# Performance work log

Hardware: AMD Instinct MI355X
Metric: run time of the kernel (lower is better)

The kernel has to match this reference:

```python
import jax, jax.numpy as jnp
import numpy as np
from jax import lax

DN = ('NCHW', 'OIHW', 'NCHW')


def conv3x3(x, w, b):
    return lax.conv_general_dilated(x, w, (1, 1), 'SAME', dimension_numbers=DN) + b[None, :, None, None]


def conv1x1(x, w, b):
    # w: [O, I] -> pointwise conv
    return jnp.einsum('oi,bihw->bohw', w, x) + b[None, :, None, None]


def sft(x0, x1, sc0w, sc0b, sc1w, sc1b, sh0w, sh0b, sh1w, sh1b):
    scale = conv1x1(jax.nn.leaky_relu(conv1x1(x1, sc0w, sc0b), 0.1), sc1w, sc1b)
    shift = conv1x1(jax.nn.leaky_relu(conv1x1(x1, sh0w, sh0b), 0.1), sh1w, sh1b)
    return x0 * (scale + 1.0) + shift


def deform_conv(x, offset, w, b):
    # torchvision DeformConv2d, 3x3, stride 1, pad 1, dilation 1, no mask.
    B, C, H, W = x.shape
    O = w.shape[0]
    K = 9
    off = offset.reshape(B, K, 2, H, W)  # (dy, dx) per kernel tap
    ki = jnp.arange(3, dtype=x.dtype) - 1.0
    ky = jnp.repeat(ki, 3)  # [9]
    kx = jnp.tile(ki, 3)
    hh = jnp.arange(H, dtype=x.dtype)
    ww = jnp.arange(W, dtype=x.dtype)
    py = off[:, :, 0] + hh[None, None, :, None] + ky[None, :, None, None]  # [B,K,H,W]
    px = off[:, :, 1] + ww[None, None, None, :] + kx[None, :, None, None]
    y0f = jnp.floor(py)
    x0f = jnp.floor(px)
    wy = (py - y0f)[:, None]  # [B,1,K,H,W]
    wx = (px - x0f)[:, None]
    y0 = y0f.astype(jnp.int32)
    x0i = x0f.astype(jnp.int32)
    x_flat = x.reshape(B, C, H * W)

    def gather(iy, ix):
        valid = (iy >= 0) & (iy < H) & (ix >= 0) & (ix < W)
        idx = (jnp.clip(iy, 0, H - 1) * W + jnp.clip(ix, 0, W - 1)).reshape(B, K * H * W)
        vals = jax.vmap(lambda xf, ii: xf[:, ii])(x_flat, idx)  # [B,C,K*H*W]
        return vals.reshape(B, C, K, H, W) * valid[:, None].astype(x.dtype)

    v00 = gather(y0, x0i)
    v01 = gather(y0, x0i + 1)
    v10 = gather(y0 + 1, x0i)
    v11 = gather(y0 + 1, x0i + 1)
    samp = (v00 * (1 - wy) * (1 - wx) + v01 * (1 - wy) * wx
            + v10 * wy * (1 - wx) + v11 * wy * wx)  # [B,C,K,H,W]
    return jnp.einsum('bckhw,ock->bohw', samp, w.reshape(O, C, K)) + b[None, :, None, None]


def setup_inputs() -> dict:
    key = jax.random.key(0)
    ks = jax.random.split(key, 32)
    B, C0, C1, H, W = 4, 128, 32, 96, 96
    f32 = jnp.float32
    d = {
        'x0': jax.random.normal(ks[0], (B, C0, H, W), f32),
        'x1': jax.random.normal(ks[1], (B, C1, H, W), f32),
        'w_off': jax.random.normal(ks[2], (18, C0, 3, 3), f32) * 0.02,
        'b_off': jnp.zeros((18,), f32),
        's1_sc0_w': jax.random.normal(ks[3], (C0, C1), f32) * 0.05,
        's1_sc0_b': jnp.zeros((C0,), f32),
        's1_sc1_w': jax.random.normal(ks[4], (C0, C0), f32) * 0.05,
        's1_sc1_b': jnp.zeros((C0,), f32),
        's1_sh0_w': jax.random.normal(ks[5], (C0, C1), f32) * 0.05,
        's1_sh0_b': jnp.zeros((C0,), f32),
        's1_sh1_w': jax.random.normal(ks[6], (C0, C0), f32) * 0.05,
        's1_sh1_b': jnp.zeros((C0,), f32),
        'w_d1': jax.random.normal(ks[7], (C0, C0, 3, 3), f32) * 0.03,
        'b_d1': jnp.zeros((C0,), f32),
        's2_sc0_w': jax.random.normal(ks[8], (C0, C1), f32) * 0.05,
        's2_sc0_b': jnp.zeros((C0,), f32),
        's2_sc1_w': jax.random.normal(ks[9], (C0, C0), f32) * 0.05,
        's2_sc1_b': jnp.zeros((C0,), f32),
        's2_sh0_w': jax.random.normal(ks[10], (C0, C1), f32) * 0.05,
        's2_sh0_b': jnp.zeros((C0,), f32),
        's2_sh1_w': jax.random.normal(ks[11], (C0, C0), f32) * 0.05,
        's2_sh1_b': jnp.zeros((C0,), f32),
        'w_d2': jax.random.normal(ks[12], (C0, C0, 3, 3), f32) * 0.03,
        'b_d2': jnp.zeros((C0,), f32),
    }
    return d


def reference(x0, x1, w_off, b_off,
              s1_sc0_w, s1_sc0_b, s1_sc1_w, s1_sc1_b,
              s1_sh0_w, s1_sh0_b, s1_sh1_w, s1_sh1_b,
              w_d1, b_d1,
              s2_sc0_w, s2_sc0_b, s2_sc1_w, s2_sc1_b,
              s2_sh0_w, s2_sh0_b, s2_sh1_w, s2_sh1_b,
              w_d2, b_d2):
    off = conv3x3(x0, w_off, b_off)
    fea = sft(x0, x1, s1_sc0_w, s1_sc0_b, s1_sc1_w, s1_sc1_b,
              s1_sh0_w, s1_sh0_b, s1_sh1_w, s1_sh1_b)
    fea = jax.nn.relu(deform_conv(fea, off, w_d1, b_d1))
    fea = sft(fea, x1, s2_sc0_w, s2_sc0_b, s2_sc1_w, s2_sc1_b,
              s2_sh0_w, s2_sh0_b, s2_sh1_w, s2_sh1_b)
    fea = deform_conv(fea, off, w_d2, b_d2)
    return x0 + fea
```

## Files before the change

### kernel.cpp

```cpp
#include <hip/hip_runtime.h>

typedef unsigned short u16;
typedef unsigned int   u32;
typedef __attribute__((ext_vector_type(8))) _Float16 f16x8;
typedef __attribute__((ext_vector_type(2))) float f32x2;
typedef __attribute__((ext_vector_type(4))) float f32x4;
typedef __attribute__((ext_vector_type(4))) unsigned int u32x4;

constexpr int B_  = 4;
constexpr int C0  = 128;
constexpr int C1  = 32;
constexpr int H_  = 96;
constexpr int W_  = 96;
constexpr int HW  = H_ * W_;
constexpr int PT  = 64;
constexpr int TPB = HW / PT;
constexpr int NTILE = B_ * TPB;

__device__ inline u16 f2h(float f) {
    _Float16 h = (_Float16)f;
    return __builtin_bit_cast(u16, h);
}

__global__ __launch_bounds__(256) void k_prep(
    const float* __restrict__ w_off,
    const float* __restrict__ wd1,  const float* __restrict__ wd2,
    const float* __restrict__ s1c0, const float* __restrict__ s1h0,
    const float* __restrict__ s2c0, const float* __restrict__ s2h0,
    const float* __restrict__ s1c1, const float* __restrict__ s1h1,
    const float* __restrict__ s2c1, const float* __restrict__ s2h1,
    float* __restrict__ wofft, u16* __restrict__ wdhi, u16* __restrict__ wdlo,
    u16* __restrict__ w0h,     u16* __restrict__ w1h)
{
    int t = blockIdx.x * 256 + threadIdx.x;
    if (t < C0 * 18 * 9) {
        int c = t / 162, r = t % 162, o = r / 9, tap = r % 9;
        wofft[t] = w_off[(o * C0 + c) * 9 + tap];
    }
    if (t < 2 * 9 * C0 * C0) {
        int d = t / (9 * C0 * C0), r = t % (9 * C0 * C0);
        int k = r / (C0 * C0), r2 = r % (C0 * C0), o = r2 / C0, c = r2 % C0;
        const float* wsrc = d ? wd2 : wd1;
        float wv = wsrc[(o * C0 + c) * 9 + k];
        _Float16 hi = (_Float16)wv;
        float rr = wv - (float)hi;
        wdhi[t] = __builtin_bit_cast(u16, hi);
        wdlo[t] = f2h(rr);
    }
    if (t < 4 * C0 * C1) {
        int m = t / (C0 * C1), i = t % (C0 * C1);
        const float* s = (m == 0) ? s1c0 : (m == 1) ? s1h0 : (m == 2) ? s2c0 : s2h0;
        w0h[t] = f2h(s[i]);
    }
    if (t < 4 * C0 * C0) {
        int m = t / (C0 * C0), i = t % (C0 * C0);
        const float* s = (m == 0) ? s1c1 : (m == 1) ? s1h1 : (m == 2) ? s2c1 : s2h1;
        w1h[t] = f2h(s[i]);
    }
}

__global__ __launch_bounds__(256) void k_conv_off(
    const float* __restrict__ x0, const float* __restrict__ wofft,
    const float* __restrict__ boff, float* __restrict__ off)
{
    int bx = blockIdx.x;
    int b  = bx / TPB;
    int p0 = (bx % TPB) * PT;
    int tid = threadIdx.x;
    int p   = tid & 63;
    int cq  = __builtin_amdgcn_readfirstlane(tid >> 6);
    int pos = p0 + p;
    int h = pos / W_, w = pos % W_;

    float acc[18];
#pragma unroll
    for (int o = 0; o < 18; ++o) acc[o] = 0.f;

    for (int cc = 0; cc < 32; ++cc) {
        int c = cq * 32 + cc;
        const float* xb = x0 + ((size_t)(b * C0 + c)) * HW;
        float v[9];
#pragma unroll
        for (int t = 0; t < 9; ++t) {
            int dy = t / 3 - 1, dx = t % 3 - 1;
            int hy = h + dy, wx = w + dx;
            bool ok = (hy >= 0) & (hy < H_) & (wx >= 0) & (wx < W_);
            v[t] = ok ? xb[hy * W_ + wx] : 0.f;
        }
        const float* wr = wofft + c * 162;
#pragma unroll
        for (int o = 0; o < 18; ++o)
#pragma unroll
            for (int t = 0; t < 9; ++t)
                acc[o] = fmaf(wr[o * 9 + t], v[t], acc[o]);
    }

    __shared__ float red[4][18][PT];
#pragma unroll
    for (int o = 0; o < 18; ++o) red[cq][o][p] = acc[o];
    __syncthreads();
    for (int idx = tid; idx < 18 * PT; idx += 256) {
        int o = idx / PT, pp = idx % PT;
        float s = red[0][o][pp] + red[1][o][pp] + red[2][o][pp] + red[3][o][pp]
                + boff[o];
        off[((size_t)(b * 18 + o)) * HW + p0 + pp] = s;
    }
}

template <int XSRC>
__global__ __launch_bounds__(512) void k_sft_mma(
    const float* __restrict__ xf,
    const float* __restrict__ xT,
    const float* __restrict__ x1,
    const u16* __restrict__ w0s, const u16* __restrict__ w0h,
    const u16* __restrict__ w1s, const u16* __restrict__ w1h,
    const float* __restrict__ b0s, const float* __restrict__ b0h,
    const float* __restrict__ b1s, const float* __restrict__ b1h,
    float* __restrict__ outT)
{
    __shared__ __align__(16) u16   x1t[64 * 32];
    __shared__ __align__(16) u16   hidt[2][64 * 128];
    __shared__ __align__(16) float outt[64 * 128];

    int bx = blockIdx.x, b = bx / TPB, p0 = (bx % TPB) * PT;
    int tid = threadIdx.x, l = tid & 63;
    int w = __builtin_amdgcn_readfirstlane(tid >> 6);
    f32x4 zz = {0.f, 0.f, 0.f, 0.f};

    for (int i = tid; i < C1 * PT; i += 512) {
        int ch = i >> 6, pos = i & 63;
        float v = x1[((size_t)(b * C1 + ch)) * HW + p0 + pos];
        x1t[pos * 32 + (ch ^ ((pos & 3) << 3))] = f2h(v);
    }
    __syncthreads();

    {
        int mt = w & 3, br = w >> 2;
        int pos = mt * 16 + (l & 15);
        int koff = (l >> 4) * 8;
        f16x8 a = *(const f16x8*)&x1t[pos * 32 + (koff ^ ((pos & 3) << 3))];
        const u16* w0 = br ? w0h : w0s;
        const float* bb = br ? b0h : b0s;
        u16* hrow = hidt[br];
#pragma unroll
        for (int nt = 0; nt < 8; ++nt) {
            int n = nt * 16 + (l & 15);
            f16x8 bfr = *(const f16x8*)&w0[n * 32 + koff];
            f32x4 h = __builtin_amdgcn_mfma_f32_16x16x32_f16(a, bfr, zz, 0, 0, 0);
            float bv = bb[n];
#pragma unroll
            for (int r = 0; r < 4; ++r) {
                float hv = h[r] + bv;
                hv = hv > 0.f ? hv : 0.1f * hv;
                int prow = mt * 16 + (l >> 4) * 4 + r;
                hrow[prow * 128 + (n ^ ((prow & 7) << 3))] = f2h(hv);
            }
        }
    }
    __syncthreads();

    f32x4 accS[4], accH[4];
#pragma unroll
    for (int nt = 0; nt < 4; ++nt) { accS[nt] = zz; accH[nt] = zz; }
    int mt = w & 3, nh = w >> 2;
    int pos = mt * 16 + (l & 15);
#pragma unroll
    for (int ks = 0; ks < 4; ++ks) {
        int kb = ks * 32 + (l >> 4) * 8;
        f16x8 aS = *(const f16x8*)&hidt[0][pos * 128 + (kb ^ ((pos & 7) << 3))];
        f16x8 aH = *(const f16x8*)&hidt[1][pos * 128 + (kb ^ ((pos & 7) << 3))];
#pragma unroll
        for (int nt = 0; nt < 4; ++nt) {
            int n = nh * 64 + nt * 16 + (l & 15);
            f16x8 bS = *(const f16x8*)&w1s[n * 128 + kb];
            f16x8 bH = *(const f16x8*)&w1h[n * 128 + kb];
            accS[nt] = __builtin_amdgcn_mfma_f32_16x16x32_f16(aS, bS, accS[nt], 0, 0, 0);
            accH[nt] = __builtin_amdgcn_mfma_f32_16x16x32_f16(aH, bH, accH[nt], 0, 0, 0);
        }
    }

#pragma unroll
    for (int nt = 0; nt < 4; ++nt) {
        int n = nh * 64 + nt * 16 + (l & 15);
        float scb = b1s[n], shb = b1h[n];
        float xv[4];
        if (XSRC == 0) {
            const float* xp = xf + ((size_t)(b * C0 + n)) * HW + p0 + mt * 16 + (l >> 4) * 4;
            f32x4 x4 = *(const f32x4*)xp;
#pragma unroll
            for (int r = 0; r < 4; ++r) xv[r] = x4[r];
        } else {
#pragma unroll
            for (int r = 0; r < 4; ++r)
                xv[r] = xT[((size_t)(b * HW + p0 + mt * 16 + (l >> 4) * 4 + r)) * C0 + n];
        }
#pragma unroll
        for (int r = 0; r < 4; ++r) {
            float scale = accS[nt][r] + scb + 1.f;
            float shift = accH[nt][r] + shb;
            outt[(mt * 16 + (l >> 4) * 4 + r) * 128 + n] = xv[r] * scale + shift;
        }
    }
    __syncthreads();

    float* dst = outT + ((size_t)(b * HW + p0)) * C0;
    for (int i = tid; i < 2048; i += 512)
        *(f32x4*)&dst[i * 4] = *(const f32x4*)&outt[i * 4];
}

template <int MODE>
__global__ __launch_bounds__(512) void k_deform3(
    const float* __restrict__ srcT,
    const float* __restrict__ off,
    const u16* __restrict__ whi,
    const u16* __restrict__ wlo,
    const float* __restrict__ bias,
    const float* __restrict__ x0,
    float* __restrict__ outF,
    float* __restrict__ outT)
{
    __shared__ __align__(16) u16 sm[4][64 * 128];
    u16* a_hi = sm[0];  u16* a_lo = sm[1];
    u16* b_hi = sm[2];  u16* b_lo = sm[3];

    int bx = blockIdx.x;
    bx = (bx & 7) * (NTILE / 8) + (bx >> 3);
    int b = bx / TPB, p0 = (bx % TPB) * PT;
    int tid = threadIdx.x, l = tid & 63;
    int w = __builtin_amdgcn_readfirstlane(tid >> 6);
    f32x4 zz = {0.f, 0.f, 0.f, 0.f};

    f32x4 acc[2][2];
#pragma unroll
    for (int hf = 0; hf < 2; ++hf)
#pragma unroll
        for (int nt = 0; nt < 2; ++nt) acc[hf][nt] = zz;

    int mt = w & 3, ng = w >> 2;
    int pos_r = mt * 16 + (l & 15);
    const float* base = srcT + (size_t)b * HW * C0;
    int so = tid >> 3, sp = tid & 7;

    for (int k = 0; k < 9; ++k) {
        for (int i = 0; i < 8; ++i) {
            int pp = w * 8 + i;
            int pos = p0 + pp;
            int h = pos / W_, wc = pos % W_;
            float dy = off[((size_t)(b * 18 + 2 * k)) * HW + pos];
            float dx = off[((size_t)(b * 18 + 2 * k + 1)) * HW + pos];
            float py = dy + (float)(h + k / 3 - 1);
            float px = dx + (float)(wc + k % 3 - 1);
            float yf = floorf(py), xf = floorf(px);
            int y0 = (int)yf, x0i = (int)xf;
            float wy = py - yf, wx = px - xf;
            bool vy0 = (y0 >= 0) & (y0 < H_), vy1 = (y0 + 1 >= 0) & (y0 + 1 < H_);
            bool vx0 = (x0i >= 0) & (x0i < W_), vx1 = (x0i + 1 >= 0) & (x0i + 1 < W_);
            float w00 = (vy0 & vx0) ? (1.f - wy) * (1.f - wx) : 0.f;
            float w01 = (vy0 & vx1) ? (1.f - wy) * wx         : 0.f;
            float w10 = (vy1 & vx0) ? wy * (1.f - wx)         : 0.f;
            float w11 = (vy1 & vx1) ? wy * wx                 : 0.f;
            int iy0 = min(max(y0, 0), H_ - 1), iy1 = min(max(y0 + 1, 0), H_ - 1);
            int ix0 = min(max(x0i, 0), W_ - 1), ix1 = min(max(x0i + 1, 0), W_ - 1);
            const float* q00 = base + (size_t)(iy0 * W_ + ix0) * C0 + 2 * l;
            const float* q01 = base + (size_t)(iy0 * W_ + ix1) * C0 + 2 * l;
            const float* q10 = base + (size_t)(iy1 * W_ + ix0) * C0 + 2 * l;
            const float* q11 = base + (size_t)(iy1 * W_ + ix1) * C0 + 2 * l;
            f32x2 v00 = *(const f32x2*)q00;
            f32x2 v01 = *(const f32x2*)q01;
            f32x2 v10 = *(const f32x2*)q10;
            f32x2 v11 = *(const f32x2*)q11;
            float s0 = v00[0] * w00 + v01[0] * w01 + v10[0] * w10 + v11[0] * w11;
            float s1 = v00[1] * w00 + v01[1] * w01 + v10[1] * w10 + v11[1] * w11;
            _Float16 h0 = (_Float16)s0, h1 = (_Float16)s1;
            float r0 = s0 - (float)h0, r1 = s1 - (float)h1;
            u32 hv = (u32)__builtin_bit_cast(u16, h0) | ((u32)__builtin_bit_cast(u16, h1) << 16);
            u32 lv = (u32)f2h(r0) | ((u32)f2h(r1) << 16);
            int ci = (2 * l) ^ ((pp & 7) << 3);
            *(u32*)&a_hi[pp * 128 + ci] = hv;
            *(u32*)&a_lo[pp * 128 + ci] = lv;
        }

#pragma unroll
        for (int hf = 0; hf < 2; ++hf) {
            {
                int orow = hf * 64 + so;
                const u16* sh = whi + ((size_t)k * C0 + orow) * C0 + sp * 16;
                const u16* sl = wlo + ((size_t)k * C0 + orow) * C0 + sp * 16;
                int sw = (so & 7) << 3;
#pragma unroll
                for (int j = 0; j < 2; ++j) {
                    int cj = (sp * 16 + j * 8) ^ sw;
                    *(u32x4*)&b_hi[so * 128 + cj] = *(const u32x4*)&sh[j * 8];
                    *(u32x4*)&b_lo[so * 128 + cj] = *(const u32x4*)&sl[j * 8];
                }
            }
            __syncthreads();
#pragma unroll
            for (int ks = 0; ks < 4; ++ks) {
                int kb = ks * 32 + (l >> 4) * 8;
                int ai = pos_r * 128 + (kb ^ ((pos_r & 7) << 3));
                f16x8 ah = *(const f16x8*)&a_hi[ai];
                f16x8 al = *(const f16x8*)&a_lo[ai];
#pragma unroll
                for (int nt = 0; nt < 2; ++nt) {
                    int orow = ng * 32 + nt * 16 + (l & 15);
                    int bi = orow * 128 + (kb ^ ((orow & 7) << 3));
                    f16x8 bh = *(const f16x8*)&b_hi[bi];
                    f16x8 bl = *(const f16x8*)&b_lo[bi];
                    acc[hf][nt] = __builtin_amdgcn_mfma_f32_16x16x32_f16(ah, bh, acc[hf][nt], 0, 0, 0);
                    acc[hf][nt] = __builtin_amdgcn_mfma_f32_16x16x32_f16(al, bh, acc[hf][nt], 0, 0, 0);
                    acc[hf][nt] = __builtin_amdgcn_mfma_f32_16x16x32_f16(ah, bl, acc[hf][nt], 0, 0, 0);
                }
            }
            __syncthreads();
        }
    }

    if (MODE == 0) {
        float* otile = (float*)sm;
#pragma unroll
        for (int hf = 0; hf < 2; ++hf)
#pragma unroll
            for (int nt = 0; nt < 2; ++nt) {
                int o = hf * 64 + ng * 32 + nt * 16 + (l & 15);
                float bv = bias[o];
#pragma unroll
                for (int r = 0; r < 4; ++r) {
                    float v = acc[hf][nt][r] + bv;
                    v = v > 0.f ? v : 0.f;
                    otile[(mt * 16 + (l >> 4) * 4 + r) * 128 + o] = v;
                }
            }
        __syncthreads();
        float* dst = outT + ((size_t)(b * HW + p0)) * C0;
        for (int i = tid; i < 2048; i += 512)
            *(f32x4*)&dst[i * 4] = *(const f32x4*)&otile[i * 4];
    } else {
#pragma unroll
        for (int hf = 0; hf < 2; ++hf)
#pragma unroll
            for (int nt = 0; nt < 2; ++nt) {
                int o = hf * 64 + ng * 32 + nt * 16 + (l & 15);
                float bv = bias[o];
                size_t base_o = ((size_t)(b * C0 + o)) * HW + p0 + mt * 16 + (l >> 4) * 4;
                f32x4 x4 = *(const f32x4*)(x0 + base_o);
                f32x4 ov;
#pragma unroll
                for (int r = 0; r < 4; ++r) ov[r] = acc[hf][nt][r] + bv + x4[r];
                *(f32x4*)(outF + base_o) = ov;
            }
    }
}

constexpr size_t WB_OFF   = 0;
constexpr size_t WB_WOFFT = 2654208;
constexpr size_t WB_W0H   = 2737152;
constexpr size_t WB_W1H   = 2769920;
constexpr size_t WB_WDHI  = 2900992;
constexpr size_t WB_WDLO  = 4080640;
constexpr size_t WB_TA    = 5260288;
constexpr size_t WB_TB    = 24134656;

extern "C" void kernel_launch(void* const* d_in, const int* in_sizes, int n_in,
                              void* d_out, int out_size, void* d_ws, size_t ws_size,
                              hipStream_t stream)
{
    const float* x0      = (const float*)d_in[0];
    const float* x1      = (const float*)d_in[1];
    const float* w_off   = (const float*)d_in[2];
    const float* b_off   = (const float*)d_in[3];
    const float* s1_sc0w = (const float*)d_in[4];
    const float* s1_sc0b = (const float*)d_in[5];
    const float* s1_sc1w = (const float*)d_in[6];
    const float* s1_sc1b = (const float*)d_in[7];
    const float* s1_sh0w = (const float*)d_in[8];
    const float* s1_sh0b = (const float*)d_in[9];
    const float* s1_sh1w = (const float*)d_in[10];
    const float* s1_sh1b = (const float*)d_in[11];
    const float* w_d1    = (const float*)d_in[12];
    const float* b_d1    = (const float*)d_in[13];
    const float* s2_sc0w = (const float*)d_in[14];
    const float* s2_sc0b = (const float*)d_in[15];
    const float* s2_sc1w = (const float*)d_in[16];
    const float* s2_sc1b = (const float*)d_in[17];
    const float* s2_sh0w = (const float*)d_in[18];
    const float* s2_sh0b = (const float*)d_in[19];
    const float* s2_sh1w = (const float*)d_in[20];
    const float* s2_sh1b = (const float*)d_in[21];
    const float* w_d2    = (const float*)d_in[22];
    const float* b_d2    = (const float*)d_in[23];

    char* wsb = (char*)d_ws;
    float* off   = (float*)(wsb + WB_OFF);
    float* wofft = (float*)(wsb + WB_WOFFT);
    u16*   w0h   = (u16*)(wsb + WB_W0H);
    u16*   w1h   = (u16*)(wsb + WB_W1H);
    u16*   wdhi  = (u16*)(wsb + WB_WDHI);
    u16*   wdlo  = (u16*)(wsb + WB_WDLO);
    float* TA    = (float*)(wsb + WB_TA);
    float* TB    = (float*)(wsb + WB_TB);

    k_prep<<<1152, 256, 0, stream>>>(w_off, w_d1, w_d2,
                                     s1_sc0w, s1_sh0w, s2_sc0w, s2_sh0w,
                                     s1_sc1w, s1_sh1w, s2_sc1w, s2_sh1w,
                                     wofft, wdhi, wdlo, w0h, w1h);
    k_conv_off<<<NTILE, 256, 0, stream>>>(x0, wofft, b_off, off);
    k_sft_mma<0><<<NTILE, 512, 0, stream>>>(x0, nullptr, x1,
                                            w0h, w0h + 4096,
                                            w1h, w1h + 16384,
                                            s1_sc0b, s1_sh0b, s1_sc1b, s1_sh1b, TA);
    k_deform3<0><<<NTILE, 512, 0, stream>>>(TA, off, wdhi, wdlo, b_d1,
                                            nullptr, nullptr, TB);
    k_sft_mma<1><<<NTILE, 512, 0, stream>>>(nullptr, TB, x1,
                                            w0h + 8192, w0h + 12288,
                                            w1h + 32768, w1h + 49152,
                                            s2_sc0b, s2_sh0b, s2_sc1b, s2_sh1b, TA);
    k_deform3<1><<<NTILE, 512, 0, stream>>>(TA, off, wdhi + 9 * 16384, wdlo + 9 * 16384,
                                            b_d2, x0, (float*)d_out, nullptr);
}
```

Before: 402.3 us.

## Precompute deform sampling indices and prefetch next tap's gathers during MFMA

The deformable conv kernel now precomputes bilinear corner indices, validity flags and fractional weights for all 9 taps into shared memory once per tile. The gathers for the next tap are issued into registers before the current tap's MFMA work, so global gather latency overlaps with matrix math. The XOR swizzle is replaced by padded row strides (136 halves, 132 floats) to avoid LDS bank conflicts, and launch bounds request 4 waves per SIMD. The cost is heavier register use (64 float2 prefetch values per thread) and more LDS per block, which can reduce occupancy or cause spills.

Result: faster. 373.3 us (-7.2%).

```diff
diff --git a/kernel.cpp b/kernel.cpp
--- a/kernel.cpp
+++ b/kernel.cpp
@@ -209,7 +209,7 @@
 }
 
 template <int MODE>
-__global__ __launch_bounds__(512) void k_deform3(
+__global__ __launch_bounds__(512, 4) void k_deform4(
     const float* __restrict__ srcT,
     const float* __restrict__ off,
     const u16* __restrict__ whi,
@@ -219,9 +219,14 @@
     float* __restrict__ outF,
     float* __restrict__ outT)
 {
-    __shared__ __align__(16) u16 sm[4][64 * 128];
-    u16* a_hi = sm[0];  u16* a_lo = sm[1];
-    u16* b_hi = sm[2];  u16* b_lo = sm[3];
+    constexpr int S = 136;
+    __shared__ __align__(16) u16   smem[4 * 64 * S];
+    __shared__ __align__(16) u16   cidx[9 * 64 * 4];
+    __shared__ __align__(16) float cwt[9 * 64 * 2];
+    u16* a_hi = smem;
+    u16* a_lo = smem + 64 * S;
+    u16* b_hi = smem + 2 * 64 * S;
+    u16* b_lo = smem + 3 * 64 * S;
 
     int bx = blockIdx.x;
     bx = (bx & 7) * (NTILE / 8) + (bx >> 3);
@@ -230,6 +235,28 @@
     int w = __builtin_amdgcn_readfirstlane(tid >> 6);
     f32x4 zz = {0.f, 0.f, 0.f, 0.f};
 
+    for (int e = tid; e < 9 * 64; e += 512) {
+        int k = e >> 6, pp = e & 63;
+        int pos = p0 + pp, h = pos / W_, wc = pos % W_;
+        float dy = off[((size_t)(b * 18 + 2 * k)) * HW + pos];
+        float dx = off[((size_t)(b * 18 + 2 * k + 1)) * HW + pos];
+        float py = dy + (float)(h + k / 3 - 1);
+        float px = dx + (float)(wc + k % 3 - 1);
+        float yf = floorf(py), xf = floorf(px);
+        int y0 = (int)yf, x0i = (int)xf;
+        cwt[e * 2]     = py - yf;
+        cwt[e * 2 + 1] = px - xf;
+        int iy0 = min(max(y0, 0), H_ - 1),     iy1 = min(max(y0 + 1, 0), H_ - 1);
+        int ix0 = min(max(x0i, 0), W_ - 1),    ix1 = min(max(x0i + 1, 0), W_ - 1);
+        bool vy0 = (y0 >= 0) & (y0 < H_),      vy1 = (y0 + 1 >= 0) & (y0 + 1 < H_);
+        bool vx0 = (x0i >= 0) & (x0i < W_),    vx1 = (x0i + 1 >= 0) & (x0i + 1 < W_);
+        cidx[e * 4 + 0] = (u16)(iy0 * W_ + ix0) | ((vy0 & vx0) ? 0x8000 : 0);
+        cidx[e * 4 + 1] = (u16)(iy0 * W_ + ix1) | ((vy0 & vx1) ? 0x8000 : 0);
+        cidx[e * 4 + 2] = (u16)(iy1 * W_ + ix0) | ((vy1 & vx0) ? 0x8000 : 0);
+        cidx[e * 4 + 3] = (u16)(iy1 * W_ + ix1) | ((vy1 & vx1) ? 0x8000 : 0);
+    }
+    __syncthreads();
+
     f32x4 acc[2][2];
 #pragma unroll
     for (int hf = 0; hf < 2; ++hf)
@@ -238,86 +265,108 @@
 
     int mt = w & 3, ng = w >> 2;
     int pos_r = mt * 16 + (l & 15);
-    const float* base = srcT + (size_t)b * HW * C0;
     int so = tid >> 3, sp = tid & 7;
-
+    const float* base  = srcT + (size_t)b * HW * C0;
+    const float* lbase = base + 2 * l;
+
+    f32x2 gv[8][4];
+
+#define ISSUE(KK)                                                             \
+    {                                                                         \
+        int ek = (KK) * 64 + w * 8;                                           \
+        _Pragma("unroll")                                                     \
+        for (int i = 0; i < 8; ++i) {                                         \
+            int e = ek + i;                                                   \
+            u32 c01 = *(const u32*)&cidx[e * 4];                              \
+            u32 c23 = *(const u32*)&cidx[e * 4 + 2];                          \
+            gv[i][0] = *(const f32x2*)(lbase + (size_t)(c01 & 0x3fffu) * C0); \
+            gv[i][1] = *(const f32x2*)(lbase + (size_t)((c01 >> 16) & 0x3fffu) * C0); \
+            gv[i][2] = *(const f32x2*)(lbase + (size_t)(c23 & 0x3fffu) * C0); \
+            gv[i][3] = *(const f32x2*)(lbase + (size_t)((c23 >> 16) & 0x3fffu) * C0); \
+        }                                                                     \
+    }
+
+#define COMMIT(KK)                                                            \
+    {                                                                         \
+        int ek = (KK) * 64 + w * 8;                                           \
+        _Pragma("unroll")                                                     \
+        for (int i = 0; i < 8; ++i) {                                         \
+            int e = ek + i, pp = w * 8 + i;                                   \
+            u32 c01 = *(const u32*)&cidx[e * 4];                              \
+            u32 c23 = *(const u32*)&cidx[e * 4 + 2];                          \
+            float wy = cwt[e * 2], wx = cwt[e * 2 + 1];                       \
+            float aa  = wy * wx;                                              \
+            float w11 = (c23 & 0x80000000u) ? aa : 0.f;                       \
+            float w10 = (c23 & 0x8000u) ? (wy - aa) : 0.f;                    \
+            float w01 = (c01 & 0x80000000u) ? (wx - aa) : 0.f;                \
+            float w00 = (c01 & 0x8000u) ? (1.f - wy - wx + aa) : 0.f;         \
+            float s0 = gv[i][0][0] * w00 + gv[i][1][0] * w01                  \
+                     + gv[i][2][0] * w10 + gv[i][3][0] * w11;                 \
+            float s1 = gv[i][0][1] * w00 + gv[i][1][1] * w01                  \
+                     + gv[i][2][1] * w10 + gv[i][3][1] * w11;                 \
+            _Float16 h0 = (_Float16)s0, h1 = (_Float16)s1;                    \
+            float r0 = s0 - (float)h0, r1 = s1 - (float)h1;                   \
+            u32 hv = (u32)__builtin_bit_cast(u16, h0)                         \
+                   | ((u32)__builtin_bit_cast(u16, h1) << 16);                \
+            u32 lv = (u32)f2h(r0) | ((u32)f2h(r1) << 16);                     \
+            *(u32*)&a_hi[pp * S + 2 * l] = hv;                                \
+            *(u32*)&a_lo[pp * S + 2 * l] = lv;                                \
+        }                                                                     \
+    }
+
+#define STAGEB(KK, HF)                                                        \
+    {                                                                         \
+        int orow = (HF) * 64 + so;                                            \
+        const u16* sh = whi + ((size_t)(KK) * C0 + orow) * C0 + sp * 16;      \
+        const u16* sl = wlo + ((size_t)(KK) * C0 + orow) * C0 + sp * 16;      \
+        _Pragma("unroll")                                                     \
+        for (int j = 0; j < 2; ++j) {                                         \
+            *(u32x4*)&b_hi[so * S + sp * 16 + j * 8] = *(const u32x4*)&sh[j * 8]; \
+            *(u32x4*)&b_lo[so * S + sp * 16 + j * 8] = *(const u32x4*)&sl[j * 8]; \
+        }                                                                     \
+    }
+
+#define MFMA_HALF(HF)                                                         \
+    {                                                                         \
+        _Pragma("unroll")                                                     \
+        for (int ks = 0; ks < 4; ++ks) {                                      \
+            int kb = ks * 32 + (l >> 4) * 8;                                  \
+            int ai = pos_r * S + kb;                                          \
+            f16x8 ah = *(const f16x8*)&a_hi[ai];                              \
+            f16x8 al = *(const f16x8*)&a_lo[ai];                              \
+            _Pragma("unroll")                                                 \
+            for (int nt = 0; nt < 2; ++nt) {                                  \
+                int orow = ng * 32 + nt * 16 + (l & 15);                      \
+                int bi = orow * S + kb;                                       \
+                f16x8 bh = *(const f16x8*)&b_hi[bi];                          \
+                f16x8 bl = *(const f16x8*)&b_lo[bi];                          \
+                acc[HF][nt] = __builtin_amdgcn_mfma_f32_16x16x32_f16(ah, bh, acc[HF][nt], 0, 0, 0); \
+                acc[HF][nt] = __builtin_amdgcn_mfma_f32_16x16x32_f16(al, bh, acc[HF][nt], 0, 0, 0); \
+                acc[HF][nt] = __builtin_amdgcn_mfma_f32_16x16x32_f16(ah, bl, acc[HF][nt], 0, 0, 0); \
+            }                                                                 \
+        }                                                                     \
+    }
+
+    ISSUE(0)
     for (int k = 0; k < 9; ++k) {
-        for (int i = 0; i < 8; ++i) {
-            int pp = w * 8 + i;
-            int pos = p0 + pp;
-            int h = pos / W_, wc = pos % W_;
-            float dy = off[((size_t)(b * 18 + 2 * k)) * HW + pos];
-            float dx = off[((size_t)(b * 18 + 2 * k + 1)) * HW + pos];
-            float py = dy + (float)(h + k / 3 - 1);
-            float px = dx + (float)(wc + k % 3 - 1);
-            float yf = floorf(py), xf = floorf(px);
-            int y0 = (int)yf, x0i = (int)xf;
-            float wy = py - yf, wx = px - xf;
-            bool vy0 = (y0 >= 0) & (y0 < H_), vy1 = (y0 + 1 >= 0) & (y0 + 1 < H_);
-            bool vx0 = (x0i >= 0) & (x0i < W_), vx1 = (x0i + 1 >= 0) & (x0i + 1 < W_);
-            float w00 = (vy0 & vx0) ? (1.f - wy) * (1.f - wx) : 0.f;
-            float w01 = (vy0 & vx1) ? (1.f - wy) * wx         : 0.f;
-            float w10 = (vy1 & vx0) ? wy * (1.f - wx)         : 0.f;
-            float w11 = (vy1 & vx1) ? wy * wx                 : 0.f;
-            int iy0 = min(max(y0, 0), H_ - 1), iy1 = min(max(y0 + 1, 0), H_ - 1);
-            int ix0 = min(max(x0i, 0), W_ - 1), ix1 = min(max(x0i + 1, 0), W_ - 1);
-            const float* q00 = base + (size_t)(iy0 * W_ + ix0) * C0 + 2 * l;
-            const float* q01 = base + (size_t)(iy0 * W_ + ix1) * C0 + 2 * l;
-            const float* q10 = base + (size_t)(iy1 * W_ + ix0) * C0 + 2 * l;
-            const float* q11 = base + (size_t)(iy1 * W_ + ix1) * C0 + 2 * l;
-            f32x2 v00 = *(const f32x2*)q00;
-            f32x2 v01 = *(const f32x2*)q01;
-            f32x2 v10 = *(const f32x2*)q10;
-            f32x2 v11 = *(const f32x2*)q11;
-            float s0 = v00[0] * w00 + v01[0] * w01 + v10[0] * w10 + v11[0] * w11;
-            float s1 = v00[1] * w00 + v01[1] * w01 + v10[1] * w10 + v11[1] * w11;
-            _Float16 h0 = (_Float16)s0, h1 = (_Float16)s1;
-            float r0 = s0 - (float)h0, r1 = s1 - (float)h1;
-            u32 hv = (u32)__builtin_bit_cast(u16, h0) | ((u32)__builtin_bit_cast(u16, h1) << 16);
-            u32 lv = (u32)f2h(r0) | ((u32)f2h(r1) << 16);
-            int ci = (2 * l) ^ ((pp & 7) << 3);
-            *(u32*)&a_hi[pp * 128 + ci] = hv;
-            *(u32*)&a_lo[pp * 128 + ci] = lv;
-        }
-
-#pragma unroll
-        for (int hf = 0; hf < 2; ++hf) {
-            {
-                int orow = hf * 64 + so;
-                const u16* sh = whi + ((size_t)k * C0 + orow) * C0 + sp * 16;
-                const u16* sl = wlo + ((size_t)k * C0 + orow) * C0 + sp * 16;
-                int sw = (so & 7) << 3;
-#pragma unroll
-                for (int j = 0; j < 2; ++j) {
-                    int cj = (sp * 16 + j * 8) ^ sw;
-                    *(u32x4*)&b_hi[so * 128 + cj] = *(const u32x4*)&sh[j * 8];
-                    *(u32x4*)&b_lo[so * 128 + cj] = *(const u32x4*)&sl[j * 8];
-                }
-            }
-            __syncthreads();
-#pragma unroll
-            for (int ks = 0; ks < 4; ++ks) {
-                int kb = ks * 32 + (l >> 4) * 8;
-                int ai = pos_r * 128 + (kb ^ ((pos_r & 7) << 3));
-                f16x8 ah = *(const f16x8*)&a_hi[ai];
-                f16x8 al = *(const f16x8*)&a_lo[ai];
-#pragma unroll
-                for (int nt = 0; nt < 2; ++nt) {
-                    int orow = ng * 32 + nt * 16 + (l & 15);
-                    int bi = orow * 128 + (kb ^ ((orow & 7) << 3));
-                    f16x8 bh = *(const f16x8*)&b_hi[bi];
-                    f16x8 bl = *(const f16x8*)&b_lo[bi];
-                    acc[hf][nt] = __builtin_amdgcn_mfma_f32_16x16x32_f16(ah, bh, acc[hf][nt], 0, 0, 0);
-                    acc[hf][nt] = __builtin_amdgcn_mfma_f32_16x16x32_f16(al, bh, acc[hf][nt], 0, 0, 0);
-                    acc[hf][nt] = __builtin_amdgcn_mfma_f32_16x16x32_f16(ah, bl, acc[hf][nt], 0, 0, 0);
-                }
-            }
-            __syncthreads();
-        }
-    }
+        COMMIT(k)
+        STAGEB(k, 0)
+        __syncthreads();
+        if (k < 8) ISSUE(k + 1)
+        MFMA_HALF(0)
+        __syncthreads();
+        STAGEB(k, 1)
+        __syncthreads();
+        MFMA_HALF(1)
+        __syncthreads();
+    }
+#undef ISSUE
+#undef COMMIT
+#undef STAGEB
+#undef MFMA_HALF
 
     if (MODE == 0) {
-        float* otile = (float*)sm;
+        float* otile = (float*)smem;
 #pragma unroll
         for (int hf = 0; hf < 2; ++hf)
 #pragma unroll
@@ -328,13 +377,15 @@
                 for (int r = 0; r < 4; ++r) {
                     float v = acc[hf][nt][r] + bv;
                     v = v > 0.f ? v : 0.f;
-                    otile[(mt * 16 + (l >> 4) * 4 + r) * 128 + o] = v;
+                    otile[(mt * 16 + (l >> 4) * 4 + r) * 132 + o] = v;
                 }
             }
         __syncthreads();
         float* dst = outT + ((size_t)(b * HW + p0)) * C0;
-        for (int i = tid; i < 2048; i += 512)
-            *(f32x4*)&dst[i * 4] = *(const f32x4*)&otile[i * 4];
+        for (int i = tid; i < 2048; i += 512) {
+            int row = i >> 5, c = i & 31;
+            *(f32x4*)&dst[row * 128 + c * 4] = *(const f32x4*)&otile[row * 132 + c * 4];
+        }
     } else {
 #pragma unroll
         for (int hf = 0; hf < 2; ++hf)
@@ -409,12 +460,12 @@
                                             w0h, w0h + 4096,
                                             w1h, w1h + 16384,
                                             s1_sc0b, s1_sh0b, s1_sc1b, s1_sh1b, TA);
-    k_deform3<0><<<NTILE, 512, 0, stream>>>(TA, off, wdhi, wdlo, b_d1,
+    k_deform4<0><<<NTILE, 512, 0, stream>>>(TA, off, wdhi, wdlo, b_d1,
                                             nullptr, nullptr, TB);
     k_sft_mma<1><<<NTILE, 512, 0, stream>>>(nullptr, TB, x1,
                                             w0h + 8192, w0h + 12288,
                                             w1h + 32768, w1h + 49152,
                                             s2_sc0b, s2_sh0b, s2_sc1b, s2_sh1b, TA);
-    k_deform3<1><<<NTILE, 512, 0, stream>>>(TA, off, wdhi + 9 * 16384, wdlo + 9 * 16384,
+    k_deform4<1><<<NTILE, 512, 0, stream>>>(TA, off, wdhi + 9 * 16384, wdlo + 9 * 16384,
                                             b_d2, x0, (float*)d_out, nullptr);
 }
```

## Cut LDS use in deform and SFT kernels to raise occupancy

Applied to the files above, without the earlier changes.

The deform kernel no longer stages weights in LDS; MFMA B operands are read straight from global (L2-cached) memory. Sampling indices, validity bits and fractional weights are precomputed once per tile into LDS. Each wave now covers 64 output channels, and padded strides replace XOR swizzles. The SFT kernel drops its output staging tile and writes directly to global memory. Both kernels get launch bounds of 6 waves per SIMD. The aim is lower LDS and register pressure so more blocks fit per CU. The risk is heavier global traffic for weights and uncoalesced SFT stores.

Measured after the change: 636.7 us. 58.3% more time.

```diff
diff --git a/kernel.cpp b/kernel.cpp
--- a/kernel.cpp
+++ b/kernel.cpp
@@ -108,7 +108,7 @@
 }
 
 template <int XSRC>
-__global__ __launch_bounds__(512) void k_sft_mma(
+__global__ __launch_bounds__(512, 6) void k_sft_mma(
     const float* __restrict__ xf,
     const float* __restrict__ xT,
     const float* __restrict__ x1,
@@ -118,9 +118,8 @@
     const float* __restrict__ b1s, const float* __restrict__ b1h,
     float* __restrict__ outT)
 {
-    __shared__ __align__(16) u16   x1t[64 * 32];
-    __shared__ __align__(16) u16   hidt[2][64 * 128];
-    __shared__ __align__(16) float outt[64 * 128];
+    __shared__ __align__(16) u16 x1t[64 * 32];
+    __shared__ __align__(16) u16 hidt[2][64 * 128];
 
     int bx = blockIdx.x, b = bx / TPB, p0 = (bx % TPB) * PT;
     int tid = threadIdx.x, l = tid & 63;
@@ -198,18 +197,14 @@
         for (int r = 0; r < 4; ++r) {
             float scale = accS[nt][r] + scb + 1.f;
             float shift = accH[nt][r] + shb;
-            outt[(mt * 16 + (l >> 4) * 4 + r) * 128 + n] = xv[r] * scale + shift;
-        }
-    }
-    __syncthreads();
-
-    float* dst = outT + ((size_t)(b * HW + p0)) * C0;
-    for (int i = tid; i < 2048; i += 512)
-        *(f32x4*)&dst[i * 4] = *(const f32x4*)&outt[i * 4];
+            outT[((size_t)(b * HW + p0 + mt * 16 + (l >> 4) * 4 + r)) * C0 + n]
+                = xv[r] * scale + shift;
+        }
+    }
 }
 
 template <int MODE>
-__global__ __launch_bounds__(512) void k_deform3(
+__global__ __launch_bounds__(512, 6) void k_deform6(
     const float* __restrict__ srcT,
     const float* __restrict__ off,
     const u16* __restrict__ whi,
@@ -219,9 +214,12 @@
     float* __restrict__ outF,
     float* __restrict__ outT)
 {
-    __shared__ __align__(16) u16 sm[4][64 * 128];
-    u16* a_hi = sm[0];  u16* a_lo = sm[1];
-    u16* b_hi = sm[2];  u16* b_lo = sm[3];
+    constexpr int S = 136;
+    __shared__ __align__(16) u16   asm_[2 * 64 * S];
+    __shared__ __align__(16) u16   cidx[9 * 64 * 4];
+    __shared__ __align__(16) float cwt[9 * 64 * 2];
+    u16* a_hi = asm_;
+    u16* a_lo = asm_ + 64 * S;
 
     int bx = blockIdx.x;
     bx = (bx & 7) * (NTILE / 8) + (bx >> 3);
@@ -230,125 +228,115 @@
     int w = __builtin_amdgcn_readfirstlane(tid >> 6);
     f32x4 zz = {0.f, 0.f, 0.f, 0.f};
 
-    f32x4 acc[2][2];
-#pragma unroll
-    for (int hf = 0; hf < 2; ++hf)
-#pragma unroll
-        for (int nt = 0; nt < 2; ++nt) acc[hf][nt] = zz;
+    for (int e = tid; e < 9 * 64; e += 512) {
+        int k = e >> 6, pp = e & 63;
+        int pos = p0 + pp, h = pos / W_, wc = pos % W_;
+        float dy = off[((size_t)(b * 18 + 2 * k)) * HW + pos];
+        float dx = off[((size_t)(b * 18 + 2 * k + 1)) * HW + pos];
+        float py = dy + (float)(h + k / 3 - 1);
+        float px = dx + (float)(wc + k % 3 - 1);
+        float yf = floorf(py), xf = floorf(px);
+        int y0 = (int)yf, x0i = (int)xf;
+        cwt[e * 2]     = py - yf;
+        cwt[e * 2 + 1] = px - xf;
+        int iy0 = min(max(y0, 0), H_ - 1),     iy1 = min(max(y0 + 1, 0), H_ - 1);
+        int ix0 = min(max(x0i, 0), W_ - 1),    ix1 = min(max(x0i + 1, 0), W_ - 1);
+        bool vy0 = (y0 >= 0) & (y0 < H_),      vy1 = (y0 + 1 >= 0) & (y0 + 1 < H_);
+        bool vx0 = (x0i >= 0) & (x0i < W_),    vx1 = (x0i + 1 >= 0) & (x0i + 1 < W_);
+        cidx[e * 4 + 0] = (u16)(iy0 * W_ + ix0) | ((vy0 & vx0) ? 0x8000 : 0);
+        cidx[e * 4 + 1] = (u16)(iy0 * W_ + ix1) | ((vy0 & vx1) ? 0x8000 : 0);
+        cidx[e * 4 + 2] = (u16)(iy1 * W_ + ix0) | ((vy1 & vx0) ? 0x8000 : 0);
+        cidx[e * 4 + 3] = (u16)(iy1 * W_ + ix1) | ((vy1 & vx1) ? 0x8000 : 0);
+    }
+    __syncthreads();
+
+    f32x4 acc[4];
+#pragma unroll
+    for (int ot = 0; ot < 4; ++ot) acc[ot] = zz;
 
     int mt = w & 3, ng = w >> 2;
     int pos_r = mt * 16 + (l & 15);
-    const float* base = srcT + (size_t)b * HW * C0;
-    int so = tid >> 3, sp = tid & 7;
+    const float* lbase = srcT + (size_t)b * HW * C0 + 2 * l;
 
     for (int k = 0; k < 9; ++k) {
+#pragma unroll
         for (int i = 0; i < 8; ++i) {
-            int pp = w * 8 + i;
-            int pos = p0 + pp;
-            int h = pos / W_, wc = pos % W_;
-            float dy = off[((size_t)(b * 18 + 2 * k)) * HW + pos];
-            float dx = off[((size_t)(b * 18 + 2 * k + 1)) * HW + pos];
-            float py = dy + (float)(h + k / 3 - 1);
-            float px = dx + (float)(wc + k % 3 - 1);
-            float yf = floorf(py), xf = floorf(px);
-            int y0 = (int)yf, x0i = (int)xf;
-            float wy = py - yf, wx = px - xf;
-            bool vy0 = (y0 >= 0) & (y0 < H_), vy1 = (y0 + 1 >= 0) & (y0 + 1 < H_);
-            bool vx0 = (x0i >= 0) & (x0i < W_), vx1 = (x0i + 1 >= 0) & (x0i + 1 < W_);
-            float w00 = (vy0 & vx0) ? (1.f - wy) * (1.f - wx) : 0.f;
-            float w01 = (vy0 & vx1) ? (1.f - wy) * wx         : 0.f;
-            float w10 = (vy1 & vx0) ? wy * (1.f - wx)         : 0.f;
-            float w11 = (vy1 & vx1) ? wy * wx                 : 0.f;
-            int iy0 = min(max(y0, 0), H_ - 1), iy1 = min(max(y0 + 1, 0), H_ - 1);
-            int ix0 = min(max(x0i, 0), W_ - 1), ix1 = min(max(x0i + 1, 0), W_ - 1);
-            const float* q00 = base + (size_t)(iy0 * W_ + ix0) * C0 + 2 * l;
-            const float* q01 = base + (size_t)(iy0 * W_ + ix1) * C0 + 2 * l;
-            const float* q10 = base + (size_t)(iy1 * W_ + ix0) * C0 + 2 * l;
-            const float* q11 = base + (size_t)(iy1 * W_ + ix1) * C0 + 2 * l;
-            f32x2 v00 = *(const f32x2*)q00;
-            f32x2 v01 = *(const f32x2*)q01;
-            f32x2 v10 = *(const f32x2*)q10;
-            f32x2 v11 = *(const f32x2*)q11;
-            float s0 = v00[0] * w00 + v01[0] * w01 + v10[0] * w10 + v11[0] * w11;
-            float s1 = v00[1] * w00 + v01[1] * w01 + v10[1] * w10 + v11[1] * w11;
+            int pp = w * 8 + i, e = k * 64 + pp;
+            u32 c01 = *(const u32*)&cidx[e * 4];
+            u32 c23 = *(const u32*)&cidx[e * 4 + 2];
+            f32x2 v0 = *(const f32x2*)(lbase + (size_t)(c01 & 0x3fffu) * C0);
+            f32x2 v1 = *(const f32x2*)(lbase + (size_t)((c01 >> 16) & 0x3fffu) * C0);
+            f32x2 v2 = *(const f32x2*)(lbase + (size_t)(c23 & 0x3fffu) * C0);
+            f32x2 v3 = *(const f32x2*)(lbase + (size_t)((c23 >> 16) & 0x3fffu) * C0);
+            float wy = cwt[e * 2], wx = cwt[e * 2 + 1];
+            float aa  = wy * wx;
+            float w11 = (c23 & 0x80000000u) ? aa : 0.f;
+            float w10 = (c23 & 0x8000u) ? (wy - aa) : 0.f;
+            float w01 = (c01 & 0x80000000u) ? (wx - aa) : 0.f;
+            float w00 = (c01 & 0x8000u) ? (1.f - wy - wx + aa) : 0.f;
+            float s0 = v0[0] * w00 + v1[0] * w01 + v2[0] * w10 + v3[0] * w11;
+            float s1 = v0[1] * w00 + v1[1] * w01 + v2[1] * w10 + v3[1] * w11;
             _Float16 h0 = (_Float16)s0, h1 = (_Float16)s1;
             float r0 = s0 - (float)h0, r1 = s1 - (float)h1;
-            u32 hv = (u32)__builtin_bit_cast(u16, h0) | ((u32)__builtin_bit_cast(u16, h1) << 16);
+            u32 hv = (u32)__builtin_bit_cast(u16, h0)
+                   | ((u32)__builtin_bit_cast(u16, h1) << 16);
             u32 lv = (u32)f2h(r0) | ((u32)f2h(r1) << 16);
-            int ci = (2 * l) ^ ((pp & 7) << 3);
-            *(u32*)&a_hi[pp * 128 + ci] = hv;
-            *(u32*)&a_lo[pp * 128 + ci] = lv;
-        }
-
-#pragma unroll
-        for (int hf = 0; hf < 2; ++hf) {
-            {
-                int orow = hf * 64 + so;
-                const u16* sh = whi + ((size_t)k * C0 + orow) * C0 + sp * 16;
-                const u16* sl = wlo + ((size_t)k * C0 + orow) * C0 + sp * 16;
-                int sw = (so & 7) << 3;
-#pragma unroll
-                for (int j = 0; j < 2; ++j) {
-                    int cj = (sp * 16 + j * 8) ^ sw;
-                    *(u32x4*)&b_hi[so * 128 + cj] = *(const u32x4*)&sh[j * 8];
-                    *(u32x4*)&b_lo[so * 128 + cj] = *(const u32x4*)&sl[j * 8];
-                }
+            *(u32*)&a_hi[pp * S + 2 * l] = hv;
+            *(u32*)&a_lo[pp * S + 2 * l] = lv;
+        }
+        __syncthreads();
+
+#pragma unroll
+        for (int ks = 0; ks < 4; ++ks) {
+            int kb = ks * 32 + (l >> 4) * 8;
+            int ai = pos_r * S + kb;
+            f16x8 ah = *(const f16x8*)&a_hi[ai];
+            f16x8 al = *(const f16x8*)&a_lo[ai];
+#pragma unroll
+            for (int ot = 0; ot < 4; ++ot) {
+                int orow = ng * 64 + ot * 16 + (l & 15);
+                size_t wi = ((size_t)k * C0 + orow) * C0 + kb;
+                f16x8 bh = *(const f16x8*)&whi[wi];
+                f16x8 bl = *(const f16x8*)&wlo[wi];
+                acc[ot] = __builtin_amdgcn_mfma_f32_16x16x32_f16(ah, bh, acc[ot], 0, 0, 0);
+                acc[ot] = __builtin_amdgcn_mfma_f32_16x16x32_f16(al, bh, acc[ot], 0, 0, 0);
+                acc[ot] = __builtin_amdgcn_mfma_f32_16x16x32_f16(ah, bl, acc[ot], 0, 0, 0);
             }
-            __syncthreads();
-#pragma unroll
-            for (int ks = 0; ks < 4; ++ks) {
-                int kb = ks * 32 + (l >> 4) * 8;
-                int ai = pos_r * 128 + (kb ^ ((pos_r & 7) << 3));
-                f16x8 ah = *(const f16x8*)&a_hi[ai];
-                f16x8 al = *(const f16x8*)&a_lo[ai];
-#pragma unroll
-                for (int nt = 0; nt < 2; ++nt) {
-                    int orow = ng * 32 + nt * 16 + (l & 15);
-                    int bi = orow * 128 + (kb ^ ((orow & 7) << 3));
-                    f16x8 bh = *(const f16x8*)&b_hi[bi];
-                    f16x8 bl = *(const f16x8*)&b_lo[bi];
-                    acc[hf][nt] = __builtin_amdgcn_mfma_f32_16x16x32_f16(ah, bh, acc[hf][nt], 0, 0, 0);
-                    acc[hf][nt] = __builtin_amdgcn_mfma_f32_16x16x32_f16(al, bh, acc[hf][nt], 0, 0, 0);
-                    acc[hf][nt] = __builtin_amdgcn_mfma_f32_16x16x32_f16(ah, bl, acc[hf][nt], 0, 0, 0);
-                }
+        }
+        __syncthreads();
+    }
+
+    if (MODE == 0) {
+        float* otile = (float*)asm_;
+#pragma unroll
+        for (int ot = 0; ot < 4; ++ot) {
+            int o = ng * 64 + ot * 16 + (l & 15);
+            float bv = bias[o];
+#pragma unroll
+            for (int r = 0; r < 4; ++r) {
+                float v = acc[ot][r] + bv;
+                v = v > 0.f ? v : 0.f;
+                otile[(mt * 16 + (l >> 4) * 4 + r) * 132 + o] = v;
             }
-            __syncthreads();
-        }
-    }
-
-    if (MODE == 0) {
-        float* otile = (float*)sm;
-#pragma unroll
-        for (int hf = 0; hf < 2; ++hf)
-#pragma unroll
-            for (int nt = 0; nt < 2; ++nt) {
-                int o = hf * 64 + ng * 32 + nt * 16 + (l & 15);
-                float bv = bias[o];
-#pragma unroll
-                for (int r = 0; r < 4; ++r) {
-                    float v = acc[hf][nt][r] + bv;
-                    v = v > 0.f ? v : 0.f;
-                    otile[(mt * 16 + (l >> 4) * 4 + r) * 128 + o] = v;
-                }
-            }
+        }
         __syncthreads();
         float* dst = outT + ((size_t)(b * HW + p0)) * C0;
-        for (int i = tid; i < 2048; i += 512)
-            *(f32x4*)&dst[i * 4] = *(const f32x4*)&otile[i * 4];
+        for (int i = tid; i < 2048; i += 512) {
+            int row = i >> 5, c = i & 31;
+            *(f32x4*)&dst[row * 128 + c * 4] = *(const f32x4*)&otile[row * 132 + c * 4];
+        }
     } else {
 #pragma unroll
-        for (int hf = 0; hf < 2; ++hf)
-#pragma unroll
-            for (int nt = 0; nt < 2; ++nt) {
-                int o = hf * 64 + ng * 32 + nt * 16 + (l & 15);
-                float bv = bias[o];
-                size_t base_o = ((size_t)(b * C0 + o)) * HW + p0 + mt * 16 + (l >> 4) * 4;
-                f32x4 x4 = *(const f32x4*)(x0 + base_o);
-                f32x4 ov;
-#pragma unroll
-                for (int r = 0; r < 4; ++r) ov[r] = acc[hf][nt][r] + bv + x4[r];
-                *(f32x4*)(outF + base_o) = ov;
-            }
+        for (int ot = 0; ot < 4; ++ot) {
+            int o = ng * 64 + ot * 16 + (l & 15);
+            float bv = bias[o];
+            size_t base_o = ((size_t)(b * C0 + o)) * HW + p0 + mt * 16 + (l >> 4) * 4;
+            f32x4 x4 = *(const f32x4*)(x0 + base_o);
+            f32x4 ov;
+#pragma unroll
+            for (int r = 0; r < 4; ++r) ov[r] = acc[ot][r] + bv + x4[r];
+            *(f32x4*)(outF + base_o) = ov;
+        }
     }
 }
 
@@ -409,12 +397,12 @@
                                             w0h, w0h + 4096,
                                             w1h, w1h + 16384,
                                             s1_sc0b, s1_sh0b, s1_sc1b, s1_sh1b, TA);
-    k_deform3<0><<<NTILE, 512, 0, stream>>>(TA, off, wdhi, wdlo, b_d1,
+    k_deform6<0><<<NTILE, 512, 0, stream>>>(TA, off, wdhi, wdlo, b_d1,
                                             nullptr, nullptr, TB);
     k_sft_mma<1><<<NTILE, 512, 0, stream>>>(nullptr, TB, x1,
                                             w0h + 8192, w0h + 12288,
                                             w1h + 32768, w1h + 49152,
                                             s2_sc0b, s2_sh0b, s2_sc1b, s2_sh1b, TA);
-    k_deform3<1><<<NTILE, 512, 0, stream>>>(TA, off, wdhi + 9 * 16384, wdlo + 9 * 16384,
+    k_deform6<1><<<NTILE, 512, 0, stream>>>(TA, off, wdhi + 9 * 16384, wdlo + 9 * 16384,
                                             b_d2, x0, (float*)d_out, nullptr);
 }
```
